# Performance work log

Measured on AMD Instinct MI355X. Metric: run time of the kernel, lower is better.

The kernel has to match this reference:

```python
import jax, jax.numpy as jnp
import numpy as np

N = 131072
C = 8
W = 256


def setup_inputs() -> dict:
    key = jax.random.key(0)
    ks = jax.random.split(key, 10)
    s1 = 1.0 / np.sqrt(3.0)
    sw = 1.0 / np.sqrt(W)
    return {
        "positions": jax.random.normal(ks[0], (N, 3), dtype=jnp.float32),
        "times": jax.random.randint(ks[1], (N,), 0, C, dtype=jnp.int64),
        "W1": jax.random.normal(ks[2], (C, 3, W), dtype=jnp.float32) * s1,
        "b1": jnp.zeros((C, W), dtype=jnp.float32),
        "W2": jax.random.normal(ks[3], (C, W, W), dtype=jnp.float32) * sw,
        "b2": jnp.zeros((C, W), dtype=jnp.float32),
        "W3": jax.random.normal(ks[4], (C, W, W), dtype=jnp.float32) * sw,
        "b3": jnp.zeros((C, W), dtype=jnp.float32),
        "W4": jax.random.normal(ks[5], (C, W, 3), dtype=jnp.float32) * sw,
        "b4": jnp.zeros((C, 3), dtype=jnp.float32),
    }


def _mlp(x, w1, c1, w2, c2, w3, c3, w4, c4):
    # 4-layer MLP, Tanh hidden activations and Tanh output activation
    h = jnp.tanh(x @ w1 + c1)
    h = jnp.tanh(h @ w2 + c2)
    h = jnp.tanh(h @ w3 + c3)
    return jnp.tanh(h @ w4 + c4)


def reference(positions, times, W1, b1, W2, b2, W3, b3, W4, b4):
    # offsets = zeros_like(positions); offsets[times==i] = mlp_i(positions[times==i])
    # classes partition the points, so this equals a per-class select-sum.
    offsets = jnp.zeros_like(positions)
    for i in range(C):  # small fixed class count
        out_i = _mlp(positions, W1[i], b1[i], W2[i], b2[i], W3[i], b3[i], W4[i], b4[i])
        mask = (times == i)[:, None]  # [N,1]
        offsets = jnp.where(mask, out_i, offsets)
    return offsets
```

## Files before the change

### kernel.cpp

```cpp
#include <hip/hip_runtime.h>
#include <stdint.h>

#define N_PTS 131072
#define NCLS 8
#define MT 64
#define CAP 32768
#define PS 2.8853900817779268f

typedef __bf16 bf16x8 __attribute__((ext_vector_type(8)));
typedef float f32x4 __attribute__((ext_vector_type(4)));

__device__ __forceinline__ float exp2_fast(float a) {
#if __has_builtin(__builtin_amdgcn_exp2f)
  return __builtin_amdgcn_exp2f(a);
#else
  return exp2f(a);
#endif
}

__device__ __forceinline__ float tanh_p2(float a) {
  return fmaf(-2.0f, __builtin_amdgcn_rcpf(exp2_fast(a) + 1.0f), 1.0f);
}

__device__ __forceinline__ unsigned short f2bf_rne(float f) {
  unsigned u = __float_as_uint(f);
  u = u + 0x7fffu + ((u >> 16) & 1u);
  return (unsigned short)(u >> 16);
}

__device__ __forceinline__ unsigned pack_bf16(float a, float b) {
  unsigned ua = __float_as_uint(a) + 0x8000u;
  unsigned ub = __float_as_uint(b) + 0x8000u;
  return __builtin_amdgcn_perm(ub, ua, 0x07060302u);
}

#define PK2_BLKS 512
#define MISC_BLKS 177
#define MISC_N 45184
#define SCAT_BLKS 512
#define PREP_GRID (PK2_BLKS + MISC_BLKS + SCAT_BLKS)

__global__ __launch_bounds__(256) void k_prep(
    const int* __restrict__ times,
    const float* __restrict__ W1, const float* __restrict__ b1,
    const float* __restrict__ W2, const float* __restrict__ b2,
    const float* __restrict__ W3, const float* __restrict__ b3,
    const float* __restrict__ W4, const float* __restrict__ b4,
    int* __restrict__ hdr, int* __restrict__ sortedIdx,
    unsigned short* __restrict__ packed23,
    float* __restrict__ w1p, float* __restrict__ b2p,
    float* __restrict__ b3p, float* __restrict__ b4p,
    unsigned short* __restrict__ W4p) {
  __shared__ int lh[NCLS], lbase[NCLS];

  int b = blockIdx.x;
  int tid = threadIdx.x;

  if (b < PK2_BLKS) {
    int cl = b >> 5;
    int k8 = b & 31;
    int j = tid;
    int l = cl >> 3, c = cl & 7;
    const float* W = (l ? W3 : W2) + c * 65536 + k8 * 8 * 256 + j;
    float v0 = W[0],        v1 = W[256],     v2 = W[2 * 256], v3 = W[3 * 256];
    float v4 = W[4 * 256],  v5 = W[5 * 256], v6 = W[6 * 256], v7 = W[7 * 256];
    uint4 pk;
    pk.x = (unsigned)f2bf_rne(PS * v0) | ((unsigned)f2bf_rne(PS * v1) << 16);
    pk.y = (unsigned)f2bf_rne(PS * v2) | ((unsigned)f2bf_rne(PS * v3) << 16);
    pk.z = (unsigned)f2bf_rne(PS * v4) | ((unsigned)f2bf_rne(PS * v5) << 16);
    pk.w = (unsigned)f2bf_rne(PS * v6) | ((unsigned)f2bf_rne(PS * v7) << 16);
    *(uint4*)&packed23[cl * 65536 + (k8 * 256 + j) * 8] = pk;
  } else if (b < PK2_BLKS + MISC_BLKS) {
    int e2 = (b - PK2_BLKS) * 256 + tid;
    if (e2 < 8192) {
      int c = e2 >> 10, rem = e2 & 1023;
      int j = rem >> 2, t = rem & 3;
      float v = (t < 3) ? W1[c * 768 + t * 256 + j] : b1[c * 256 + j];
      w1p[e2] = PS * v;
    } else if (e2 < 10240) {
      int i = e2 - 8192;
      b2p[i] = PS * b2[i];
    } else if (e2 < 12288) {
      int i = e2 - 10240;
      b3p[i] = PS * b3[i];
    } else if (e2 < 12416) {
      int i = e2 - 12288;
      int c = i >> 4, r = i & 15;
      b4p[i] = (r < 3) ? PS * b4[c * 3 + r] : 0.0f;
    } else if (e2 < MISC_N) {
      int i = e2 - 12416;
      int c = i >> 12, rem = i & 4095;
      int jj = rem & 7, j = (rem >> 3) & 15, k = ((rem >> 7) << 3) + jj;
      float v = (j < 3) ? PS * W4[c * 768 + k * 3 + j] : 0.0f;
      W4p[c * 4096 + rem] = f2bf_rne(v);
    }
  } else {
    int sb = b - (PK2_BLKS + MISC_BLKS);
    if (tid < NCLS) lh[tid] = 0;
    __syncthreads();
    int i = sb * 256 + tid;
    int t = times[i];
    int r = atomicAdd(&lh[t], 1);
    __syncthreads();
    if (tid < NCLS) lbase[tid] = lh[tid] ? atomicAdd(&hdr[tid], lh[tid]) : 0;
    __syncthreads();
    sortedIdx[t * CAP + lbase[t] + r] = i;
  }
}

__device__ __forceinline__ void mfma_layer16(
    unsigned short (*__restrict__ Abuf)[MT][8],
    const bf16x8* __restrict__ Af,
    const float* __restrict__ biasp,
    int tid) {
  int lane = tid & 63, w = tid >> 6;
  int quad = lane >> 4, l16 = lane & 15;
  int jbase = w * 64;

  f32x4 acc[4][4];
#pragma unroll
  for (int jf = 0; jf < 4; jf++) {
    f32x4 bv = *(const f32x4*)&biasp[jbase + jf * 16 + quad * 4];
#pragma unroll
    for (int mt = 0; mt < 4; mt++) acc[jf][mt] = bv;
  }

#pragma unroll
  for (int kb = 0; kb < 8; kb++) {
    int kq = kb * 4 + quad;
    bf16x8 af[4], bfr[4];
#pragma unroll
    for (int jf = 0; jf < 4; jf++)
      af[jf] = Af[kq * 256 + jbase + jf * 16 + l16];
#pragma unroll
    for (int mt = 0; mt < 4; mt++)
      bfr[mt] = *(const bf16x8*)&Abuf[kq][mt * 16 + l16][0];
#pragma unroll
    for (int jf = 0; jf < 4; jf++)
#pragma unroll
      for (int mt = 0; mt < 4; mt++)
        acc[jf][mt] = __builtin_amdgcn_mfma_f32_16x16x32_bf16(af[jf], bfr[mt], acc[jf][mt], 0, 0, 0);
  }

  __syncthreads();

#pragma unroll
  for (int jf = 0; jf < 4; jf++) {
    int jbq = jbase + jf * 16 + quad * 4;
#pragma unroll
    for (int mt = 0; mt < 4; mt++) {
      float t0 = tanh_p2(acc[jf][mt][0]);
      float t1 = tanh_p2(acc[jf][mt][1]);
      float t2 = tanh_p2(acc[jf][mt][2]);
      float t3 = tanh_p2(acc[jf][mt][3]);
      uint2 pk = make_uint2(pack_bf16(t0, t1), pack_bf16(t2, t3));
      *(uint2*)&Abuf[jbq >> 3][mt * 16 + l16][jbq & 7] = pk;
    }
  }
}

__global__ __launch_bounds__(256, 4) void k_mlp(
    const float* __restrict__ pos,
    const int* __restrict__ hdr, const int* __restrict__ sortedIdx,
    const unsigned short* __restrict__ packed23,
    const float* __restrict__ w1p, const float* __restrict__ b2p,
    const float* __restrict__ b3p, const float* __restrict__ b4p,
    const unsigned short* __restrict__ W4p,
    float* __restrict__ out) {

  __shared__ __align__(16) unsigned short Abuf[32][MT][8];
  __shared__ __align__(16) float4 w1i[256];
  __shared__ __align__(16) float4 xpos4[MT];
  __shared__ int sIdx[MT];

  int b = blockIdx.x;
  int tid = threadIdx.x;

  int c = -1, t0 = 0, cnt = 0;
  {
    int ts = 0;
#pragma unroll
    for (int cc = 0; cc < NCLS; cc++) {
      int cc_cnt = hdr[cc];
      int tiles = (cc_cnt + MT - 1) >> 6;
      if (b >= ts && b < ts + tiles) { c = cc; t0 = b - ts; cnt = cc_cnt; }
      ts += tiles;
    }
  }
  if (c < 0) return;
  int base = c * CAP + t0 * MT;
  int mCount = min(MT, cnt - t0 * MT);

  if (tid < MT) sIdx[tid] = sortedIdx[base + min(tid, mCount - 1)];
  w1i[tid] = ((const float4*)(w1p + (size_t)c * 1024))[tid];
  __syncthreads();
  if (tid < MT) {
    int idx = sIdx[tid] * 3;
    xpos4[tid] = make_float4(pos[idx], pos[idx + 1], pos[idx + 2], 0.0f);
  }
  __syncthreads();

  {
    int m = tid & 63, q = tid >> 6;
    float4 xp = xpos4[m];
#pragma unroll
    for (int i8 = 0; i8 < 8; i8++) {
      int j8 = q * 8 + i8;
      unsigned pk[4];
#pragma unroll
      for (int jp = 0; jp < 4; jp++) {
        float t[2];
#pragma unroll
        for (int u = 0; u < 2; u++) {
          float4 wv = w1i[j8 * 8 + jp * 2 + u];
          float a = fmaf(xp.x, wv.x, fmaf(xp.y, wv.y, fmaf(xp.z, wv.z, wv.w)));
          t[u] = tanh_p2(a);
        }
        pk[jp] = pack_bf16(t[0], t[1]);
      }
      *(uint4*)&Abuf[j8][m][0] = make_uint4(pk[0], pk[1], pk[2], pk[3]);
    }
  }
  __syncthreads();

  mfma_layer16(Abuf, (const bf16x8*)(packed23 + ((size_t)c << 16)),
               b2p + c * 256, tid);
  __syncthreads();
  mfma_layer16(Abuf, (const bf16x8*)(packed23 + ((size_t)(8 + c) << 16)),
               b3p + c * 256, tid);
  __syncthreads();

  {
    int lane = tid & 63, w = tid >> 6;
    int quad = lane >> 4, l16 = lane & 15;
    f32x4 acc = *(const f32x4*)&b4p[c * 16 + quad * 4];
#pragma unroll
    for (int kb = 0; kb < 8; kb++) {
      int kq = kb * 4 + quad;
      bf16x8 a4 = *(const bf16x8*)&W4p[((size_t)c * 512 + kq * 16 + l16) * 8];
      bf16x8 b4f = *(const bf16x8*)&Abuf[kq][w * 16 + l16][0];
      acc = __builtin_amdgcn_mfma_f32_16x16x32_bf16(a4, b4f, acc, 0, 0, 0);
    }
    int m = w * 16 + l16;
    if (quad == 0 && m < mCount) {
      int o = sIdx[m] * 3;
      out[o + 0] = tanh_p2(acc[0]);
      out[o + 1] = tanh_p2(acc[1]);
      out[o + 2] = tanh_p2(acc[2]);
    }
  }
}

extern "C" void kernel_launch(void* const* d_in, const int* in_sizes, int n_in,
                              void* d_out, int out_size, void* d_ws, size_t ws_size,
                              hipStream_t stream) {
  const float* pos = (const float*)d_in[0];
  const int* times = (const int*)d_in[1];
  const float* W1 = (const float*)d_in[2];
  const float* b1 = (const float*)d_in[3];
  const float* W2 = (const float*)d_in[4];
  const float* b2 = (const float*)d_in[5];
  const float* W3 = (const float*)d_in[6];
  const float* b3 = (const float*)d_in[7];
  const float* W4 = (const float*)d_in[8];
  const float* b4 = (const float*)d_in[9];

  char* ws = (char*)d_ws;
  int* hdr = (int*)ws;
  int* sortedIdx = (int*)(ws + 4096);
  float* w1p = (float*)(ws + 1052672);
  float* b2p = (float*)(ws + 1085440);
  float* b3p = (float*)(ws + 1093632);
  float* b4p = (float*)(ws + 1101824);
  unsigned short* W4p = (unsigned short*)(ws + 1102336);
  unsigned short* packed23 = (unsigned short*)(ws + (2u << 20));
  float* out = (float*)d_out;

  hipMemsetAsync(d_ws, 0, 64, stream);
  k_prep<<<PREP_GRID, 256, 0, stream>>>(times, W1, b1, W2, b2, W3, b3, W4, b4,
                                        hdr, sortedIdx, packed23,
                                        w1p, b2p, b3p, b4p, W4p);
  k_mlp<<<N_PTS / MT + NCLS, 256, 0, stream>>>(
      pos, hdr, sortedIdx, packed23, w1p, b2p, b3p, b4p, W4p, out);
}
```

Measured before the change: 131.9 us.

## Split MLP tile into two row halves to overlap tanh epilogue with MFMA

Splits each 64-row tile into two 32-row halves and interleaves the stages. Layer-1 of the second half overlaps layer-2 MFMAs of the first half, and the tanh/bf16 epilogue of one half overlaps the MFMA loop of the other, across layers 2 and 3. Positions are now gathered directly by 192 threads instead of through sIdx, which removes one block barrier. Barrier count rises in the pipelined section, and the interleaving depends on the compiler scheduling VALU and MFMA work together without raising register pressure.

After: 145.4 us. +10.3%, slower.

```diff
diff --git a/kernel.cpp b/kernel.cpp
--- a/kernel.cpp
+++ b/kernel.cpp
@@ -108,57 +108,6 @@
   }
 }
 
-__device__ __forceinline__ void mfma_layer16(
-    unsigned short (*__restrict__ Abuf)[MT][8],
-    const bf16x8* __restrict__ Af,
-    const float* __restrict__ biasp,
-    int tid) {
-  int lane = tid & 63, w = tid >> 6;
-  int quad = lane >> 4, l16 = lane & 15;
-  int jbase = w * 64;
-
-  f32x4 acc[4][4];
-#pragma unroll
-  for (int jf = 0; jf < 4; jf++) {
-    f32x4 bv = *(const f32x4*)&biasp[jbase + jf * 16 + quad * 4];
-#pragma unroll
-    for (int mt = 0; mt < 4; mt++) acc[jf][mt] = bv;
-  }
-
-#pragma unroll
-  for (int kb = 0; kb < 8; kb++) {
-    int kq = kb * 4 + quad;
-    bf16x8 af[4], bfr[4];
-#pragma unroll
-    for (int jf = 0; jf < 4; jf++)
-      af[jf] = Af[kq * 256 + jbase + jf * 16 + l16];
-#pragma unroll
-    for (int mt = 0; mt < 4; mt++)
-      bfr[mt] = *(const bf16x8*)&Abuf[kq][mt * 16 + l16][0];
-#pragma unroll
-    for (int jf = 0; jf < 4; jf++)
-#pragma unroll
-      for (int mt = 0; mt < 4; mt++)
-        acc[jf][mt] = __builtin_amdgcn_mfma_f32_16x16x32_bf16(af[jf], bfr[mt], acc[jf][mt], 0, 0, 0);
-  }
-
-  __syncthreads();
-
-#pragma unroll
-  for (int jf = 0; jf < 4; jf++) {
-    int jbq = jbase + jf * 16 + quad * 4;
-#pragma unroll
-    for (int mt = 0; mt < 4; mt++) {
-      float t0 = tanh_p2(acc[jf][mt][0]);
-      float t1 = tanh_p2(acc[jf][mt][1]);
-      float t2 = tanh_p2(acc[jf][mt][2]);
-      float t3 = tanh_p2(acc[jf][mt][3]);
-      uint2 pk = make_uint2(pack_bf16(t0, t1), pack_bf16(t2, t3));
-      *(uint2*)&Abuf[jbq >> 3][mt * 16 + l16][jbq & 7] = pk;
-    }
-  }
-}
-
 __global__ __launch_bounds__(256, 4) void k_mlp(
     const float* __restrict__ pos,
     const int* __restrict__ hdr, const int* __restrict__ sortedIdx,
@@ -170,7 +119,7 @@
 
   __shared__ __align__(16) unsigned short Abuf[32][MT][8];
   __shared__ __align__(16) float4 w1i[256];
-  __shared__ __align__(16) float4 xpos4[MT];
+  __shared__ __align__(16) float xpos[MT][4];
   __shared__ int sIdx[MT];
 
   int b = blockIdx.x;
@@ -191,21 +140,30 @@
   int base = c * CAP + t0 * MT;
   int mCount = min(MT, cnt - t0 * MT);
 
+  int lane = tid & 63, w = tid >> 6;
+  int quad = lane >> 4, l16 = lane & 15;
+  int jbase = w * 64;
+
   if (tid < MT) sIdx[tid] = sortedIdx[base + min(tid, mCount - 1)];
+  if (tid < MT * 3) {
+    int m = tid / 3, comp = tid - 3 * m;
+    int idx = sortedIdx[base + min(m, mCount - 1)];
+    xpos[m][comp] = pos[idx * 3 + comp];
+  }
   w1i[tid] = ((const float4*)(w1p + (size_t)c * 1024))[tid];
-  __syncthreads();
-  if (tid < MT) {
-    int idx = sIdx[tid] * 3;
-    xpos4[tid] = make_float4(pos[idx], pos[idx + 1], pos[idx + 2], 0.0f);
-  }
-  __syncthreads();
-
-  {
-    int m = tid & 63, q = tid >> 6;
-    float4 xp = xpos4[m];
-#pragma unroll
-    for (int i8 = 0; i8 < 8; i8++) {
-      int j8 = q * 8 + i8;
+
+  const bf16x8* Af2 = (const bf16x8*)(packed23 + ((size_t)c << 16));
+  const bf16x8* Af3 = (const bf16x8*)(packed23 + ((size_t)(8 + c) << 16));
+  const float* bias2 = b2p + c * 256;
+  const float* bias3 = b3p + c * 256;
+
+  auto l1half = [&](int mh) {
+    int m = (tid & 31) + mh * 32;
+    int jq = tid >> 5;
+    float x0 = xpos[m][0], x1 = xpos[m][1], x2 = xpos[m][2];
+#pragma unroll
+    for (int i8 = 0; i8 < 4; i8++) {
+      int j8 = jq * 4 + i8;
       unsigned pk[4];
 #pragma unroll
       for (int jp = 0; jp < 4; jp++) {
@@ -213,26 +171,79 @@
 #pragma unroll
         for (int u = 0; u < 2; u++) {
           float4 wv = w1i[j8 * 8 + jp * 2 + u];
-          float a = fmaf(xp.x, wv.x, fmaf(xp.y, wv.y, fmaf(xp.z, wv.z, wv.w)));
+          float a = fmaf(x0, wv.x, fmaf(x1, wv.y, fmaf(x2, wv.z, wv.w)));
           t[u] = tanh_p2(a);
         }
         pk[jp] = pack_bf16(t[0], t[1]);
       }
       *(uint4*)&Abuf[j8][m][0] = make_uint4(pk[0], pk[1], pk[2], pk[3]);
     }
-  }
-  __syncthreads();
-
-  mfma_layer16(Abuf, (const bf16x8*)(packed23 + ((size_t)c << 16)),
-               b2p + c * 256, tid);
-  __syncthreads();
-  mfma_layer16(Abuf, (const bf16x8*)(packed23 + ((size_t)(8 + c) << 16)),
-               b3p + c * 256, tid);
+  };
+
+  auto pfun = [&](const bf16x8* __restrict__ Af, const float* __restrict__ biasp,
+                  int mh, f32x4 (&acc)[4][2]) {
+#pragma unroll
+    for (int jf = 0; jf < 4; jf++) {
+      f32x4 bv = *(const f32x4*)&biasp[jbase + jf * 16 + quad * 4];
+      acc[jf][0] = bv;
+      acc[jf][1] = bv;
+    }
+#pragma unroll
+    for (int kb = 0; kb < 8; kb++) {
+      int kq = kb * 4 + quad;
+      bf16x8 af[4], bfr[2];
+#pragma unroll
+      for (int jf = 0; jf < 4; jf++)
+        af[jf] = Af[kq * 256 + jbase + jf * 16 + l16];
+#pragma unroll
+      for (int mt = 0; mt < 2; mt++)
+        bfr[mt] = *(const bf16x8*)&Abuf[kq][(mh * 2 + mt) * 16 + l16][0];
+#pragma unroll
+      for (int jf = 0; jf < 4; jf++)
+#pragma unroll
+        for (int mt = 0; mt < 2; mt++)
+          acc[jf][mt] = __builtin_amdgcn_mfma_f32_16x16x32_bf16(af[jf], bfr[mt], acc[jf][mt], 0, 0, 0);
+    }
+  };
+
+  auto efun = [&](f32x4 (&acc)[4][2], int mh) {
+#pragma unroll
+    for (int jf = 0; jf < 4; jf++) {
+      int jbq = jbase + jf * 16 + quad * 4;
+#pragma unroll
+      for (int mt = 0; mt < 2; mt++) {
+        int m = (mh * 2 + mt) * 16 + l16;
+        float t0 = tanh_p2(acc[jf][mt][0]);
+        float t1 = tanh_p2(acc[jf][mt][1]);
+        float t2 = tanh_p2(acc[jf][mt][2]);
+        float t3 = tanh_p2(acc[jf][mt][3]);
+        uint2 pk = make_uint2(pack_bf16(t0, t1), pack_bf16(t2, t3));
+        *(uint2*)&Abuf[jbq >> 3][m][jbq & 7] = pk;
+      }
+    }
+  };
+
+  f32x4 accA[4][2], accB[4][2];
+
+  __syncthreads();
+  l1half(0);
+  __syncthreads();
+  l1half(1);
+  pfun(Af2, bias2, 0, accA);
+  __syncthreads();
+  pfun(Af2, bias2, 1, accB);
+  efun(accA, 0);
+  __syncthreads();
+  efun(accB, 1);
+  pfun(Af3, bias3, 0, accA);
+  __syncthreads();
+  pfun(Af3, bias3, 1, accB);
+  efun(accA, 0);
+  __syncthreads();
+  efun(accB, 1);
   __syncthreads();
 
   {
-    int lane = tid & 63, w = tid >> 6;
-    int quad = lane >> 4, l16 = lane & 15;
     f32x4 acc = *(const f32x4*)&b4p[c * 16 + quad * 4];
 #pragma unroll
     for (int kb = 0; kb < 8; kb++) {
```
